# Kernel optimization log

Hardware: AMD Instinct MI355X
Metric: run time of the kernel (lower is better)

## Reference

```python
import jax, jax.numpy as jnp
import numpy as np
import math

HEADS = 16
SPH = 64      # size_per_head
KEY = 64      # key_size (defaults to size_per_head)
EMB = 1024
STEP = 3


def extract_seq_patches(x, kernel_size, step):
    # x: [B, L, D] -> [B, L, kernel_size, D]; patch j at pos t is x_pad[t - p_left + j*step]
    B, L, D = x.shape
    k_size = kernel_size + (step - 1) * (kernel_size - 1)
    p_right = (k_size - 1) // 2
    p_left = k_size - 1 - p_right
    xp = jnp.pad(x, ((0, 0), (p_left, p_right), (0, 0)))
    xs = [xp[:, i:i + L] for i in range(0, k_size, step)]  # kernel_size slices
    return jnp.stack(xs, axis=2)


def setup_inputs() -> dict:
    key = jax.random.key(0)
    kx, kq, kk, kv = jax.random.split(key, 4)
    B, L = 2, 4096
    x = jax.random.normal(kx, (B, L, EMB), dtype=jnp.float32)
    W_q = jax.random.normal(kq, (EMB, HEADS * KEY), dtype=jnp.float32) * 0.02
    W_k = jax.random.normal(kk, (EMB, HEADS * KEY), dtype=jnp.float32) * 0.02
    W_v = jax.random.normal(kv, (EMB, HEADS * SPH), dtype=jnp.float32) * 0.02
    return {"x": x, "W_q": W_q, "W_k": W_k, "W_v": W_v}


def _forward(x, W_q, W_k, W_v):
    B, L, D = x.shape
    pad_len = STEP - L % STEP
    x = jnp.pad(x, ((0, 0), (0, pad_len), (0, 0)))
    new_len = L + pad_len
    blocks = new_len // STEP
    q = x @ W_q  # [B, new_len, H*KEY]
    k = x @ W_k
    v = x @ W_v
    ksz = 1 + 2 * (STEP - 1)  # kernel_size = 5
    kp = extract_seq_patches(k, ksz, STEP)  # [B, new_len, ksz, H*KEY]
    vp = extract_seq_patches(v, ksz, STEP)
    # reshape to [B, H, step, blocks, d]
    q = q.reshape(B, blocks, STEP, HEADS, KEY).transpose(0, 3, 2, 1, 4)
    kb = k.reshape(B, blocks, STEP, HEADS, KEY).transpose(0, 3, 2, 1, 4)
    vb = v.reshape(B, blocks, STEP, HEADS, SPH).transpose(0, 3, 2, 1, 4)
    # neighbor patches: [B, H, step, blocks, ksz, d]
    kp = kp.reshape(B, blocks, STEP, ksz, HEADS, KEY).transpose(0, 4, 2, 1, 3, 5)
    vp = vp.reshape(B, blocks, STEP, ksz, HEADS, SPH).transpose(0, 4, 2, 1, 3, 5)
    scale = 1.0 / math.sqrt(KEY)
    # strided attention over blocks (same residue mod step): [B,H,step,blocks,blocks]
    a = jnp.einsum('bhsqk,bhspk->bhsqp', q, kb) * scale
    # block-local neighbor attention: [B,H,step,blocks,ksz]
    ap = jnp.einsum('bhsqk,bhsqnk->bhsqn', q, kp) * scale
    A = jax.nn.softmax(jnp.concatenate([a, ap], axis=-1), axis=-1)
    a, ap = A[..., :blocks], A[..., blocks:]
    o = (jnp.einsum('bhsqp,bhspd->bhsqd', a, vb)
         + jnp.einsum('bhsqn,bhsqnd->bhsqd', ap, vp))
    o = o.transpose(0, 3, 2, 1, 4).reshape(B, new_len, HEADS * SPH)
    return o[:, :L]


def reference(x, W_q, W_k, W_v):
    return _forward(x, W_q, W_k, W_v)
```

## Files before the change

### kernel.cpp

```cpp
#include <hip/hip_runtime.h>
#include <hip/hip_bf16.h>

typedef unsigned int u32;
typedef unsigned short u16;
typedef short s8v __attribute__((ext_vector_type(8)));
typedef short s4v __attribute__((ext_vector_type(4)));
typedef float f4v __attribute__((ext_vector_type(4)));
typedef float f16v __attribute__((ext_vector_type(16)));
typedef u32 u32x2 __attribute__((ext_vector_type(2)));
typedef u32 u32x4 __attribute__((ext_vector_type(4)));

#define NBLK 1366
#define VROW 1376
#define QSCALE 0.18033688011112042f

__device__ __forceinline__ u16 f2b(float f) {
  u32 u = __builtin_bit_cast(u32, f);
  u = (u + 0x7FFFu + ((u >> 16) & 1u)) >> 16;
  return (u16)u;
}

__device__ __forceinline__ u32 cvtpk(float a, float b) {
  u32 r;
  asm("v_cvt_pk_bf16_f32 %0, %1, %2" : "=v"(r) : "v"(a), "v"(b));
  return r;
}

__device__ __forceinline__ float fexp2(float x) {
#if defined(__has_builtin)
#if __has_builtin(__builtin_amdgcn_exp2f)
  return __builtin_amdgcn_exp2f(x);
#define FEXP2_DONE 1
#endif
#endif
#ifndef FEXP2_DONE
  float r;
  asm("v_exp_f32 %0, %1" : "=v"(r) : "v"(x));
  return r;
#endif
}

__device__ __forceinline__ void gll16(const void* g, void* l) {
  __builtin_amdgcn_global_load_lds(
      (const __attribute__((address_space(1))) u32*)g,
      (__attribute__((address_space(3))) u32*)l, 16, 0, 0);
}

__device__ __forceinline__ f4v mfma32(s8v a, s8v b, f4v c) {
  return __builtin_amdgcn_mfma_f32_16x16x32_bf16(a, b, c, 0, 0, 0);
}

__device__ __forceinline__ f16v mfma3216(s8v a, s8v b, f16v c) {
  return __builtin_amdgcn_mfma_f32_32x32x16_bf16(a, b, c, 0, 0, 0);
}

__device__ __forceinline__ s4v lo4(s8v v) {
  return __builtin_shufflevector(v, v, 0, 1, 2, 3);
}
__device__ __forceinline__ s4v hi4(s8v v) {
  return __builtin_shufflevector(v, v, 4, 5, 6, 7);
}

__global__ __launch_bounds__(256) void k_prep(const float* __restrict__ x,
                                              const float* __restrict__ Wq,
                                              const float* __restrict__ Wk,
                                              const float* __restrict__ Wv,
                                              u16* __restrict__ xb,
                                              u16* __restrict__ Wt,
                                              u16* __restrict__ Vt) {
  const int bid = blockIdx.x;
  const int tid = threadIdx.x;
  if (bid < 4160) {
    long base = ((long)bid * 256 + tid) * 8;
    if (base >= 8320L * 1024L) return;
    int m = (int)(base >> 10);
    int c = (int)(base & 1023);
    int b = m / 4098;
    int t = m - b * 4098;
    s8v pack;
    if (m < 8196 && t < 4096) {
      const float* src = x + ((size_t)b * 4096 + t) * 1024 + c;
      float4 v0 = *(const float4*)(src);
      float4 v1 = *(const float4*)(src + 4);
      pack[0] = (short)f2b(v0.x); pack[1] = (short)f2b(v0.y);
      pack[2] = (short)f2b(v0.z); pack[3] = (short)f2b(v0.w);
      pack[4] = (short)f2b(v1.x); pack[5] = (short)f2b(v1.y);
      pack[6] = (short)f2b(v1.z); pack[7] = (short)f2b(v1.w);
    } else {
#pragma unroll
      for (int i = 0; i < 8; ++i) pack[i] = 0;
    }
    *(s8v*)(xb + base) = pack;
  } else if (bid < 7232) {
    __shared__ float tile[32][33];
    int bid3 = bid - 4160;
    int z = bid3 >> 10;
    int rem = bid3 & 1023;
    const float* W = (z == 0) ? Wq : ((z == 1) ? Wk : Wv);
    u16* dst = Wt + (size_t)z * 1024 * 1024;
    int n0 = (rem & 31) * 32, k0 = (rem >> 5) * 32;
    int tx = tid & 31, ty = tid >> 5;
#pragma unroll
    for (int i = 0; i < 4; ++i)
      tile[ty + i * 8][tx] = W[(size_t)(k0 + ty + i * 8) * 1024 + n0 + tx];
    __syncthreads();
#pragma unroll
    for (int i = 0; i < 4; ++i)
      dst[(size_t)(n0 + ty + i * 8) * 1024 + k0 + tx] = f2b(tile[tx][ty + i * 8]);
  } else {
    int gidx = (bid - 7232) * 256 + tid;
    if (gidx < 6144) {
      u16* dst = Vt + (size_t)gidx * VROW + NBLK;
#pragma unroll
      for (int i = 0; i < 10; ++i) dst[i] = 0;
    } else if (gidx < 6400) {
      Vt[(size_t)6144 * VROW + (gidx - 6144)] = 0;
    }
  }
}

__global__ __launch_bounds__(256) void k_gemm_qkv(const u16* __restrict__ xb,
                                                  const u16* __restrict__ Wt,
                                                  u16* __restrict__ Qp,
                                                  u16* __restrict__ Kp,
                                                  u16* __restrict__ Vt) {
  const int wg = blockIdx.x;
  const int wid = (wg & 7) * 195 + (wg >> 3);
  const int mt = wid / 24;
  const int nz = wid - mt * 24;
  const int zid = nz >> 3;
  const int m0 = mt * 128;
  const int n0 = (nz & 7) * 128;
  const u16* Bg = Wt + (size_t)zid * 1024 * 1024 + (size_t)n0 * 1024;

  __shared__ __align__(16) u16 shl[16384];
  u16* A0 = shl;
  u16* A1 = shl + 4096;
  u16* B0 = shl + 8192;
  u16* B1 = shl + 12288;

  const int tid = threadIdx.x;
  const int lane = tid & 63;
  const int w = tid >> 6;
  const int wr = w >> 1, wc = w & 1;
  const int lo = lane & 15, g = lane >> 4;

  const int lrow = lane >> 2;
  const int csrc = (lane & 3) ^ ((lane >> 3) & 3);
  const int rsw = (g ^ ((lo >> 1) & 3)) << 4;

  f4v acc[4][4];
#pragma unroll
  for (int i = 0; i < 4; ++i)
#pragma unroll
    for (int j = 0; j < 4; ++j) {
      f4v z = {0.f, 0.f, 0.f, 0.f};
      acc[i][j] = z;
    }

  auto stage = [&](int kt, u16* Ab, u16* Bb) {
#pragma unroll
    for (int c = 0; c < 2; ++c) {
      int rloc = w * 32 + c * 16 + lrow;
      gll16(xb + (size_t)(m0 + rloc) * 1024 + kt + csrc * 8,
            Ab + (w * 32 + c * 16) * 32);
      gll16(Bg + (size_t)rloc * 1024 + kt + csrc * 8,
            Bb + (w * 32 + c * 16) * 32);
    }
  };

  auto compute = [&](const u16* Ab, const u16* Bb) {
    s8v af[4], bf[4];
#pragma unroll
    for (int i = 0; i < 4; ++i) {
      int ar = wr * 64 + i * 16 + lo;
      af[i] = *(const s8v*)((const char*)Ab + ar * 64 + rsw);
      int br = wc * 64 + i * 16 + lo;
      bf[i] = *(const s8v*)((const char*)Bb + br * 64 + rsw);
    }
    __builtin_amdgcn_s_setprio(1);
#pragma unroll
    for (int i = 0; i < 4; ++i)
#pragma unroll
      for (int j = 0; j < 4; ++j)
        acc[i][j] = mfma32(af[i], bf[j], acc[i][j]);
    __builtin_amdgcn_s_setprio(0);
  };

#define BAR_VM4                                             \
  asm volatile("s_waitcnt vmcnt(4)" ::: "memory");          \
  __builtin_amdgcn_s_barrier();                             \
  asm volatile("" ::: "memory");
#define BAR_LGKM                                            \
  asm volatile("s_waitcnt lgkmcnt(0)" ::: "memory");        \
  __builtin_amdgcn_s_barrier();                             \
  asm volatile("" ::: "memory");

  stage(0, A0, B0);
#pragma unroll 1
  for (int kk = 0; kk < 15; ++kk) {
    int kt = kk * 64;
    stage(kt + 32, A1, B1);
    BAR_VM4
    compute(A0, B0);
    BAR_LGKM
    stage(kt + 64, A0, B0);
    BAR_VM4
    compute(A1, B1);
    BAR_LGKM
  }
  stage(31 * 32, A1, B1);
  BAR_VM4
  compute(A0, B0);
  BAR_LGKM
  asm volatile("s_waitcnt vmcnt(0)" ::: "memory");
  __builtin_amdgcn_s_barrier();
  asm volatile("" ::: "memory");
  compute(A1, B1);
  __syncthreads();

#undef BAR_VM4
#undef BAR_LGKM

  const float esc = (zid == 0) ? QSCALE : 1.0f;
  if (zid != 2) {
    u16* dq = (zid == 0) ? Qp : Kp;
#pragma unroll
    for (int i = 0; i < 4; ++i) {
#pragma unroll
      for (int r = 0; r < 4; ++r) {
        int m = m0 + wr * 64 + i * 16 + g * 4 + r;
        if (m >= 8196) continue;
        int b = m / 4098;
        int t = m - b * 4098;
        int s = t % 3;
        int p = t / 3;
        int cb = (b * 3 + s) * 16;
#pragma unroll
        for (int j = 0; j < 4; ++j) {
          int n = n0 + wc * 64 + j * 16 + lo;
          int h = n >> 6, d = n & 63;
          dq[(size_t)((cb + h) * NBLK + p) * 64 + d] = f2b(acc[i][j][r] * esc);
        }
      }
    }
  } else {
    u16* tile = shl;
#pragma unroll
    for (int i = 0; i < 4; ++i)
#pragma unroll
      for (int r = 0; r < 4; ++r) {
        int ml = wr * 64 + i * 16 + g * 4 + r;
#pragma unroll
        for (int j = 0; j < 4; ++j) {
          int nl = wc * 64 + j * 16 + lo;
          tile[ml * 128 + nl] = f2b(acc[i][j][r]);
        }
      }
    __syncthreads();
    for (int pair = tid; pair < 384; pair += 256) {
      int nl = pair & 127;
      int s = pair >> 7;
      int n = n0 + nl;
      int h = n >> 6, d = n & 63;
      for (int b = 0; b < 2; ++b) {
        int mlo = m0 > b * 4098 ? m0 : b * 4098;
        int cap = b * 4098 + 4096;
        int mhi = (m0 + 128 < cap) ? m0 + 128 : cap;
        if (mlo >= mhi) continue;
        int t_lo = mlo - b * 4098;
        int add = (s - (t_lo % 3) + 3) % 3;
        int t = t_lo + add;
        int tend = mhi - b * 4098;
        u16* dst = Vt + (size_t)(((b * 3 + s) * 16 + h) * 64 + d) * VROW;
        for (; t < tend; t += 3)
          dst[t / 3] = tile[(b * 4098 + t - m0) * 128 + nl];
      }
    }
  }
}

__global__ __launch_bounds__(256, 4) void k_attn(const u16* __restrict__ Qp,
                                                 const u16* __restrict__ Kp,
                                                 const u16* __restrict__ Vt,
                                                 float* __restrict__ out) {
  const int wg = blockIdx.x;
  const int idx = (wg & 7) * 132 + (wg >> 3);
  const int combo = idx / 11;
  const int qb = idx - combo * 11;
  const int b = combo / 48;
  const int rem = combo - b * 48;
  const int s = rem >> 4;
  const int h = rem & 15;
  const int tid = threadIdx.x, lane = tid & 63, w = tid >> 6;
  const int lq = lane & 31, lh = lane >> 5;

  const u16* Qg = Qp + (size_t)combo * (NBLK * 64);
  const u16* Kg = Kp + (size_t)combo * (NBLK * 64);
  const u16* Vg = Vt + (size_t)combo * (64 * VROW);

  __shared__ __align__(16) u16 att[2][4][64 * 36];

  const int qg = qb * 128 + w * 32 + lq;
  const int qc = (qg < NBLK) ? qg : (NBLK - 1);
  s8v qf[4];
#pragma unroll
  for (int ss = 0; ss < 4; ++ss)
    qf[ss] = *(const s8v*)(Qg + (size_t)qc * 64 + ss * 16 + lh * 8);

  f16v oacc0, oacc1;
#pragma unroll
  for (int i = 0; i < 16; ++i) { oacc0[i] = 0.f; oacc1[i] = 0.f; }
  float dpart[4] = {0.f, 0.f, 0.f, 0.f};

  const int srow = tid >> 2;
  const int sch = (tid & 3) * 2;
  const int ssub = (tid & 3) * 8;
  s8v kr0, kr1, vr0, vr1;

  auto load_regs = [&](int jt) {
    const int j0 = jt * 64;
    const u16* kp = Kg + (size_t)(j0 + srow) * 64 + sch * 8;
    kr0 = *(const s8v*)(kp);
    kr1 = *(const s8v*)(kp + 8);
    const u16* vp = Vg + (size_t)srow * VROW + j0 + sch * 8;
    vr0 = *(const s8v*)(vp);
    vr1 = *(const s8v*)(vp + 8);
  };

  auto stage_write = [&](int slot) {
    u16* K0 = att[slot][0];
    u16* K1 = att[slot][1];
    u16* V0 = att[slot][2];
    u16* V1 = att[slot][3];
    const int kb = srow * 36 + ssub;
    *(s4v*)(K0 + kb) = lo4(kr0);
    *(s4v*)(K0 + kb + 4) = hi4(kr0);
    *(s4v*)(K1 + kb) = lo4(kr1);
    *(s4v*)(K1 + kb + 4) = hi4(kr1);
    const int vb0 = srow * 36 + sch * 4;
    *(s4v*)(V0 + vb0) = lo4(vr0);
    *(s4v*)(V1 + vb0) = hi4(vr0);
    *(s4v*)(V0 + vb0 + 4) = lo4(vr1);
    *(s4v*)(V1 + vb0 + 4) = hi4(vr1);
  };

  const int qmin = qb * 128;

  auto compute = [&](int slot, int jt) {
    const int j0 = jt * 64;
    const u16* Kb = att[slot][lh];
    const u16* Vl0 = att[slot][2];
    const u16* Vl1 = att[slot][3];

    const bool special = ((j0 <= qmin + 130) && (j0 + 65 >= qmin)) || (j0 + 64 > NBLK);
#pragma unroll
    for (int jb = 0; jb < 2; ++jb) {
      f16v sacc;
#pragma unroll
      for (int i = 0; i < 16; ++i) sacc[i] = 0.f;
      __builtin_amdgcn_s_setprio(1);
#pragma unroll
      for (int ss = 0; ss < 4; ++ss) {
        const u16* kp = Kb + (jb * 32 + lq) * 36 + ss * 8;
        s4v a = *(const s4v*)kp;
        s4v b2 = *(const s4v*)(kp + 4);
        s8v kf = __builtin_shufflevector(a, b2, 0, 1, 2, 3, 4, 5, 6, 7);
        sacc = mfma3216(kf, qf[ss], sacc);
      }
      __builtin_amdgcn_s_setprio(0);

      float e[16];
      if (special) {
#pragma unroll
        for (int r = 0; r < 16; ++r) {
          int j = j0 + jb * 32 + (r & 3) + 8 * (r >> 2) + 4 * lh;
          float ev = fexp2(sacc[r]);
          int dd = j - qg;
          float fac = (j < NBLK) ? (((dd <= 2) && (dd >= -2)) ? 2.f : 1.f) : 0.f;
          e[r] = ev * fac;
        }
      } else {
#pragma unroll
        for (int r = 0; r < 16; ++r) e[r] = fexp2(sacc[r]);
      }
#pragma unroll
      for (int r = 0; r < 16; ++r) dpart[r & 3] += e[r];

#pragma unroll
      for (int g2 = 0; g2 < 2; ++g2) {
        u32 pe0 = cvtpk(e[g2 * 8 + 0], e[g2 * 8 + 1]);
        u32 pe1 = cvtpk(e[g2 * 8 + 2], e[g2 * 8 + 3]);
        u32 pe2 = cvtpk(e[g2 * 8 + 4], e[g2 * 8 + 5]);
        u32 pe3 = cvtpk(e[g2 * 8 + 6], e[g2 * 8 + 7]);
        asm("v_permlane32_swap_b32 %0, %1" : "+v"(pe0), "+v"(pe2));
        asm("v_permlane32_swap_b32 %0, %1" : "+v"(pe1), "+v"(pe3));
        u32x4 fw;
        fw[0] = pe0; fw[1] = pe1; fw[2] = pe2; fw[3] = pe3;
        s8v ef8 = __builtin_bit_cast(s8v, fw);
        const int ci = (jb * 4 + g2 * 2 + lh) * 4;
        s4v v0a = *(const s4v*)(Vl0 + lq * 36 + ci);
        s4v v0b = *(const s4v*)(Vl1 + lq * 36 + ci);
        s8v vf0 = __builtin_shufflevector(v0a, v0b, 0, 1, 2, 3, 4, 5, 6, 7);
        s4v v1a = *(const s4v*)(Vl0 + (32 + lq) * 36 + ci);
        s4v v1b = *(const s4v*)(Vl1 + (32 + lq) * 36 + ci);
        s8v vf1 = __builtin_shufflevector(v1a, v1b, 0, 1, 2, 3, 4, 5, 6, 7);
        __builtin_amdgcn_s_setprio(1);
        oacc0 = mfma3216(ef8, vf0, oacc0);
        oacc1 = mfma3216(ef8, vf1, oacc1);
        __builtin_amdgcn_s_setprio(0);
      }
    }
  };

#define LGKM_BAR                                            \
  asm volatile("s_waitcnt lgkmcnt(0)" ::: "memory");        \
  __builtin_amdgcn_s_barrier();                             \
  asm volatile("" ::: "memory");

  load_regs(0);
  stage_write(0);
  load_regs(1);
  LGKM_BAR

#pragma unroll 1
  for (int t = 0; t < 21; ++t) {
    compute(t & 1, t);
    stage_write((t + 1) & 1);
    if (t < 20) load_regs(t + 2);
    LGKM_BAR
  }
  compute(1, 21);

#undef LGKM_BAR

  float dtot = (dpart[0] + dpart[1]) + (dpart[2] + dpart[3]);
  dtot += __shfl_xor(dtot, 32, 64);

  const int hbase = h * 64;
#pragma unroll
  for (int r = 0; r < 16; ++r) {
    int cr = (r & 3) + 8 * (r >> 2) + 4 * lh;
    int q = qb * 128 + w * 32 + cr;
    float dq = __shfl(dtot, cr, 64);
    dq += (q == 0 || q == NBLK - 1) ? 2.f : ((q == 1 || q == NBLK - 2) ? 1.f : 0.f);
    float rr = 1.f / dq;
    int t = 3 * q + s;
    if (q < NBLK && t < 4096) {
      float* orow = out + ((size_t)b * 4096 + t) * 1024 + hbase + lq;
      orow[0] = oacc0[r] * rr;
      orow[32] = oacc1[r] * rr;
    }
  }
}

extern "C" void kernel_launch(void* const* d_in, const int* in_sizes, int n_in,
                              void* d_out, int out_size, void* d_ws, size_t ws_size,
                              hipStream_t stream) {
  const float* x  = (const float*)d_in[0];
  const float* Wq = (const float*)d_in[1];
  const float* Wk = (const float*)d_in[2];
  const float* Wv = (const float*)d_in[3];
  float* out = (float*)d_out;

  u16* ws = (u16*)d_ws;
  u16* xb = ws;
  u16* Wt = xb + 8519680;
  u16* Qp = Wt + 3145728;
  u16* Kp = Qp + 8392704;
  u16* Vt = Kp + 8392704;

  k_prep<<<dim3(7257), 256, 0, stream>>>(x, Wq, Wk, Wv, xb, Wt, Vt);
  k_gemm_qkv<<<dim3(1560), 256, 0, stream>>>(xb, Wt, Qp, Kp, Vt);
  k_attn<<<dim3(1056), 256, 0, stream>>>(Qp, Kp, Vt, out);
}
```

Before: 202.9 us.

## Replace direct-to-LDS loads with register-staged prefetch pipeline in QKV GEMM

The QKV projection GEMM stops using global_load_lds DMA into LDS. It now prefetches the next K-tile into registers with vector global loads, then writes them to a double-buffered LDS slot after computing the current tile, using a single barrier per iteration. Launch bounds gain a minimum of 4 blocks per CU. The aim is to cut barrier and vmcnt stalls and overlap global latency with MFMA work. The cost is extra VGPRs and explicit LDS writes, and the tighter register budget from the occupancy hint could cause spills.

```diff
diff --git a/kernel.cpp b/kernel.cpp
--- a/kernel.cpp
+++ b/kernel.cpp
@@ -38,12 +38,6 @@
   asm("v_exp_f32 %0, %1" : "=v"(r) : "v"(x));
   return r;
 #endif
-}
-
-__device__ __forceinline__ void gll16(const void* g, void* l) {
-  __builtin_amdgcn_global_load_lds(
-      (const __attribute__((address_space(1))) u32*)g,
-      (__attribute__((address_space(3))) u32*)l, 16, 0, 0);
 }
 
 __device__ __forceinline__ f4v mfma32(s8v a, s8v b, f4v c) {
@@ -119,11 +113,11 @@
   }
 }
 
-__global__ __launch_bounds__(256) void k_gemm_qkv(const u16* __restrict__ xb,
-                                                  const u16* __restrict__ Wt,
-                                                  u16* __restrict__ Qp,
-                                                  u16* __restrict__ Kp,
-                                                  u16* __restrict__ Vt) {
+__global__ __launch_bounds__(256, 4) void k_gemm_qkv(const u16* __restrict__ xb,
+                                                     const u16* __restrict__ Wt,
+                                                     u16* __restrict__ Qp,
+                                                     u16* __restrict__ Kp,
+                                                     u16* __restrict__ Vt) {
   const int wg = blockIdx.x;
   const int wid = (wg & 7) * 195 + (wg >> 3);
   const int mt = wid / 24;
@@ -134,10 +128,6 @@
   const u16* Bg = Wt + (size_t)zid * 1024 * 1024 + (size_t)n0 * 1024;
 
   __shared__ __align__(16) u16 shl[16384];
-  u16* A0 = shl;
-  u16* A1 = shl + 4096;
-  u16* B0 = shl + 8192;
-  u16* B1 = shl + 12288;
 
   const int tid = threadIdx.x;
   const int lane = tid & 63;
@@ -145,8 +135,10 @@
   const int wr = w >> 1, wc = w & 1;
   const int lo = lane & 15, g = lane >> 4;
 
-  const int lrow = lane >> 2;
-  const int csrc = (lane & 3) ^ ((lane >> 3) & 3);
+  const int srow = tid >> 1;
+  const int zsw = (tid >> 2) & 3;
+  const int s0 = (tid & 1) * 2;
+  const int c0 = s0 ^ zsw, c1 = (s0 + 1) ^ zsw;
   const int rsw = (g ^ ((lo >> 1) & 3)) << 4;
 
   f4v acc[4][4];
@@ -158,25 +150,36 @@
       acc[i][j] = z;
     }
 
-  auto stage = [&](int kt, u16* Ab, u16* Bb) {
-#pragma unroll
-    for (int c = 0; c < 2; ++c) {
-      int rloc = w * 32 + c * 16 + lrow;
-      gll16(xb + (size_t)(m0 + rloc) * 1024 + kt + csrc * 8,
-            Ab + (w * 32 + c * 16) * 32);
-      gll16(Bg + (size_t)rloc * 1024 + kt + csrc * 8,
-            Bb + (w * 32 + c * 16) * 32);
-    }
-  };
-
-  auto compute = [&](const u16* Ab, const u16* Bb) {
+  s8v ra0, ra1, rb0, rb1;
+  auto load_regs = [&](int tile) {
+    const int kt = tile * 32;
+    const u16* ap = xb + (size_t)(m0 + srow) * 1024 + kt;
+    ra0 = *(const s8v*)(ap + c0 * 8);
+    ra1 = *(const s8v*)(ap + c1 * 8);
+    const u16* bp = Bg + (size_t)srow * 1024 + kt;
+    rb0 = *(const s8v*)(bp + c0 * 8);
+    rb1 = *(const s8v*)(bp + c1 * 8);
+  };
+
+  auto stage_write = [&](int slot) {
+    u16* Ab = shl + slot * 4096;
+    u16* Bb = shl + 8192 + slot * 4096;
+    *(s8v*)(Ab + srow * 32 + s0 * 8) = ra0;
+    *(s8v*)(Ab + srow * 32 + s0 * 8 + 8) = ra1;
+    *(s8v*)(Bb + srow * 32 + s0 * 8) = rb0;
+    *(s8v*)(Bb + srow * 32 + s0 * 8 + 8) = rb1;
+  };
+
+  auto compute = [&](int slot) {
+    const char* Ab = (const char*)(shl + slot * 4096);
+    const char* Bb = (const char*)(shl + 8192 + slot * 4096);
     s8v af[4], bf[4];
 #pragma unroll
     for (int i = 0; i < 4; ++i) {
       int ar = wr * 64 + i * 16 + lo;
-      af[i] = *(const s8v*)((const char*)Ab + ar * 64 + rsw);
+      af[i] = *(const s8v*)(Ab + ar * 64 + rsw);
       int br = wc * 64 + i * 16 + lo;
-      bf[i] = *(const s8v*)((const char*)Bb + br * 64 + rsw);
+      bf[i] = *(const s8v*)(Bb + br * 64 + rsw);
     }
     __builtin_amdgcn_s_setprio(1);
 #pragma unroll
@@ -187,40 +190,27 @@
     __builtin_amdgcn_s_setprio(0);
   };
 
-#define BAR_VM4                                             \
-  asm volatile("s_waitcnt vmcnt(4)" ::: "memory");          \
-  __builtin_amdgcn_s_barrier();                             \
-  asm volatile("" ::: "memory");
-#define BAR_LGKM                                            \
+#define LGKM_BAR                                            \
   asm volatile("s_waitcnt lgkmcnt(0)" ::: "memory");        \
   __builtin_amdgcn_s_barrier();                             \
   asm volatile("" ::: "memory");
 
-  stage(0, A0, B0);
+  load_regs(0);
+  stage_write(0);
+  load_regs(1);
+  LGKM_BAR
+
 #pragma unroll 1
-  for (int kk = 0; kk < 15; ++kk) {
-    int kt = kk * 64;
-    stage(kt + 32, A1, B1);
-    BAR_VM4
-    compute(A0, B0);
-    BAR_LGKM
-    stage(kt + 64, A0, B0);
-    BAR_VM4
-    compute(A1, B1);
-    BAR_LGKM
+  for (int t = 0; t < 31; ++t) {
+    compute(t & 1);
+    stage_write((t + 1) & 1);
+    if (t < 30) load_regs(t + 2);
+    LGKM_BAR
   }
-  stage(31 * 32, A1, B1);
-  BAR_VM4
-  compute(A0, B0);
-  BAR_LGKM
-  asm volatile("s_waitcnt vmcnt(0)" ::: "memory");
-  __builtin_amdgcn_s_barrier();
-  asm volatile("" ::: "memory");
-  compute(A1, B1);
+  compute(1);
   __syncthreads();
 
-#undef BAR_VM4
-#undef BAR_LGKM
+#undef LGKM_BAR
 
   const float esc = (zid == 0) ? QSCALE : 1.0f;
   if (zid != 2) {
```

After: 209.4 us. 1.03x slower.
